# Kernel optimization log

Measured on AMD Instinct MI355X. Metric: run time of the kernel, lower is better.

The kernel has to match this reference:

```python
import jax, jax.numpy as jnp
import numpy as np

NUM_FEATURES = 1024
NUM_GROUPS = 64
NUM_POS = 3
BATCH = 8192  # rows per view; N = NUM_POS * BATCH


def setup_inputs() -> dict:
    key = jax.random.key(0)
    kx, kp = jax.random.split(key)
    x = jax.random.normal(kx, (NUM_POS * BATCH, NUM_FEATURES), dtype=jnp.float32)
    # one independent column permutation per view (deterministic stand-in for torch.randperm)
    pkeys = jax.random.split(kp, NUM_POS)
    perms = jnp.stack([jax.random.permutation(k, NUM_FEATURES) for k in pkeys]).astype(jnp.int32)
    return {"x": x, "perms": perms}


def _group_whiten(x, perms):
    # x: [N, D] with N = 3*B; perms: [3, D]
    N, D = x.shape
    B = N // NUM_POS
    G = NUM_GROUPS
    d = D // G
    xs = x.reshape(NUM_POS, B, D)                                  # [3, B, D]
    # shuffle feature columns per view: x.t()[perm].t()
    xp = jnp.take_along_axis(xs, perms[:, None, :], axis=2)        # [3, B, D]
    xg = xp.reshape(NUM_POS, B, G, d)                              # [3, B, G, d]
    xc = xg - xg.mean(axis=1, keepdims=True)                       # center over batch
    xt = xc.transpose(0, 2, 1, 3)                                  # [3, G, B, d]
    cov = jnp.einsum('sgbd,sgbe->sgde', xt, xt) / B                # [3, G, d, d]
    S, U = jnp.linalg.eigh(cov)                                    # symmetric eig (symeig)
    # W = U diag(S^-1/2) U^T
    W = jnp.einsum('sgde,sge,sgfe->sgdf', U, jax.lax.rsqrt(S), U)  # [3, G, d, d]
    y = jnp.einsum('sgbd,sgde->sgbe', xt, W)                       # [3, G, B, d]
    # unshuffle: transpose(1,2).flatten(0,1)[argsort(perm)].t()
    yf = y.transpose(0, 1, 3, 2).reshape(NUM_POS, D, B)            # [3, D, B]
    inv = jnp.argsort(perms, axis=1)                               # inverse permutation
    yu = jnp.take_along_axis(yf, inv[:, :, None], axis=1)          # [3, D, B]
    return yu.transpose(0, 2, 1).reshape(N, D)                     # [N, D]


def reference(x, perms):
    return _group_whiten(x, perms)
```

## Files before the change

kernel.cpp:

```cpp
#include <hip/hip_runtime.h>
#include <stdint.h>


constexpr int D_FEAT  = 1024;
constexpr int NGROUP  = 64;
constexpr int GD      = 16;
constexpr int NB      = 8192;
constexpr int NVIEW   = 3;

constexpr int P1      = 256;
constexpr int RPP1    = NB / P1;
constexpr int RPB3    = 32;
constexpr int C3      = 4;
constexpr int PSPLIT  = 8;
constexpr int PER     = P1 / PSPLIT;

constexpr int SXX_FLOATS  = NGROUP * GD * GD;
constexpr int PART_STRIDE = SXX_FLOATS + D_FEAT;
constexpr int PSTRIDE_U32 = PART_STRIDE / 2;
constexpr int ENT         = NVIEW * PART_STRIDE;
constexpr int ENT_DW      = NVIEW * PSTRIDE_U32;

constexpr int SX_OFF  = 0;
constexpr int W_OFF   = SX_OFF + NVIEW * D_FEAT;
constexpr int RED_OFF = W_OFF + NVIEW * SXX_FLOATS;

template <int B>
__device__ __forceinline__ float qbc(float x) {
    return __int_as_float(__builtin_amdgcn_mov_dpp(
        __float_as_int(x), B * 0x55 , 0xF, 0xF, true));
}

__device__ __forceinline__ uint32_t pkbf2(float a, float b) {
    uint32_t ua = __float_as_uint(a), ub = __float_as_uint(b);
    ua += 0x7FFFu + ((ua >> 16) & 1u);
    ub += 0x7FFFu + ((ub >> 16) & 1u);
    return (ua >> 16) | (ub & 0xFFFF0000u);
}

__global__ __launch_bounds__(256, 3) void k_stats_gather(const float* __restrict__ x,
                                                         const int* __restrict__ perms,
                                                         uint32_t* __restrict__ part) {
    const int s   = blockIdx.y;
    const int p   = blockIdx.x;
    const int tid = threadIdx.x;

    int pcolq[4];
#pragma unroll
    for (int jj = 0; jj < 4; ++jj) pcolq[jj] = perms[s * D_FEAT + tid * 4 + jj];

    float acc[GD][4];
#pragma unroll
    for (int i = 0; i < GD; ++i)
#pragma unroll
        for (int jj = 0; jj < 4; ++jj) acc[i][jj] = 0.0f;
    float sacc[4] = {0.0f, 0.0f, 0.0f, 0.0f};

    const float* xbase = x + (size_t)(s * NB + p * RPP1) * D_FEAT;

#define ROW_ACC(Q0, Q1, Q2, Q3)                                                \
    {                                                                          \
        float vq_[4] = {Q0, Q1, Q2, Q3};                                       \
        float v_[GD];                                                          \
        _Pragma("unroll")                                                      \
        for (int jj = 0; jj < 4; ++jj) {                                       \
            v_[0  + jj] = qbc<0>(vq_[jj]);                                     \
            v_[4  + jj] = qbc<1>(vq_[jj]);                                     \
            v_[8  + jj] = qbc<2>(vq_[jj]);                                     \
            v_[12 + jj] = qbc<3>(vq_[jj]);                                     \
        }                                                                      \
        _Pragma("unroll")                                                      \
        for (int jj = 0; jj < 4; ++jj) sacc[jj] += vq_[jj];                    \
        _Pragma("unroll")                                                      \
        for (int i = 0; i < GD; ++i)                                           \
            _Pragma("unroll")                                                  \
            for (int jj = 0; jj < 4; ++jj)                                     \
                acc[i][jj] = fmaf(v_[i], vq_[jj], acc[i][jj]);                 \
    }

    for (int r = 0; r < RPP1; r += 4) {
        const float* r0 = xbase + (size_t)r * D_FEAT;
        const float* r1 = r0 + D_FEAT;
        const float* r2 = r1 + D_FEAT;
        const float* r3 = r2 + D_FEAT;
        const float a0 = r0[pcolq[0]], a1 = r0[pcolq[1]],
                    a2 = r0[pcolq[2]], a3 = r0[pcolq[3]];
        const float b0 = r1[pcolq[0]], b1 = r1[pcolq[1]],
                    b2 = r1[pcolq[2]], b3 = r1[pcolq[3]];
        const float c0 = r2[pcolq[0]], c1 = r2[pcolq[1]],
                    c2 = r2[pcolq[2]], c3 = r2[pcolq[3]];
        const float d0 = r3[pcolq[0]], d1 = r3[pcolq[1]],
                    d2 = r3[pcolq[2]], d3 = r3[pcolq[3]];
        ROW_ACC(a0, a1, a2, a3)
        ROW_ACC(b0, b1, b2, b3)
        ROW_ACC(c0, c1, c2, c3)
        ROW_ACC(d0, d1, d2, d3)
    }
#undef ROW_ACC

    uint32_t* dst = part + (size_t)(s * P1 + p) * PSTRIDE_U32;
#pragma unroll
    for (int i = 0; i < GD; ++i) {
        dst[i * 512 + tid * 2 + 0] = pkbf2(acc[i][0], acc[i][1]);
        dst[i * 512 + tid * 2 + 1] = pkbf2(acc[i][2], acc[i][3]);
    }
    dst[8192 + tid * 2 + 0] = pkbf2(sacc[0], sacc[1]);
    dst[8192 + tid * 2 + 1] = pkbf2(sacc[2], sacc[3]);
}

__global__ __launch_bounds__(256) void k_reduce1(const uint32_t* __restrict__ part,
                                                 float* __restrict__ red) {
    const int fd = blockIdx.x * 256 + threadIdx.x;
    if (fd >= ENT_DW) return;
    const int s = fd / PSTRIDE_U32, ffd = fd % PSTRIDE_U32;
    const uint32_t* src =
        part + ((size_t)s * P1 + blockIdx.y * PER) * PSTRIDE_U32 + ffd;
    float s0 = 0.0f, s1 = 0.0f;
#pragma unroll 8
    for (int p = 0; p < PER; ++p) {
        const uint32_t u = src[(size_t)p * PSTRIDE_U32];
        s0 += __uint_as_float(u << 16);
        s1 += __uint_as_float(u & 0xFFFF0000u);
    }
    float* r = red + (size_t)blockIdx.y * ENT + s * PART_STRIDE + ffd * 2;
    r[0] = s0;
    r[1] = s1;
}

__global__ __launch_bounds__(256) void k_invsqrt(const float* __restrict__ red,
                                                 float* __restrict__ ws) {
    __shared__ float Ym[GD][GD];
    __shared__ float Zm[GD][GD];
    __shared__ float Tm[GD][GD];
    __shared__ float Mu[GD];
    const int bx = blockIdx.x;
    const int s = bx >> 6, g = bx & 63;
    const int tid = threadIdx.x;
    const int i = tid >> 4, j = tid & 15;
    const float invB = 1.0f / (float)NB;

    const int f_sxx = s * PART_STRIDE + i * D_FEAT + g * GD + j;
    float sxx = 0.0f;
#pragma unroll
    for (int pp = 0; pp < PSPLIT; ++pp) sxx += red[(size_t)pp * ENT + f_sxx];

    if (tid < GD) {
        const int f_sx = s * PART_STRIDE + SXX_FLOATS + g * GD + tid;
        float sx = 0.0f;
#pragma unroll
        for (int pp = 0; pp < PSPLIT; ++pp) sx += red[(size_t)pp * ENT + f_sx];
        ws[SX_OFF + s * D_FEAT + g * GD + tid] = sx;
        Mu[tid] = sx * invB;
    }
    __syncthreads();
    const float a = sxx * invB - Mu[i] * Mu[j];

    Ym[i][j] = a;
    __syncthreads();
    float tr = 0.0f;
#pragma unroll
    for (int k = 0; k < GD; ++k) tr += Ym[k][k];
    const float sc = tr * (1.0f / (float)GD);
    const float inv_sc = 1.0f / sc;
    __syncthreads();
    Ym[i][j] = a * inv_sc;
    Zm[i][j] = (i == j) ? 1.0f : 0.0f;
    __syncthreads();

    float zn = (i == j) ? 1.0f : 0.0f;
    for (int it = 0; it < 6; ++it) {
        float t = 0.0f;
#pragma unroll
        for (int k = 0; k < GD; ++k) t += Zm[i][k] * Ym[k][j];
        t = ((i == j) ? 1.5f : 0.0f) - 0.5f * t;
        Tm[i][j] = t;
        __syncthreads();
        float yn = 0.0f;
        zn = 0.0f;
#pragma unroll
        for (int k = 0; k < GD; ++k) {
            yn += Ym[i][k] * Tm[k][j];
            zn += Tm[i][k] * Zm[k][j];
        }
        __syncthreads();
        Ym[i][j] = yn;
        Zm[i][j] = zn;
        __syncthreads();
    }
    ws[W_OFF + (size_t)((s * NGROUP + g) * GD + i) * GD + j] = zn * rsqrtf(sc);
}

__global__ __launch_bounds__(256, 3) void k_apply(const float* __restrict__ x,
                                                  const int* __restrict__ perms,
                                                  const float* __restrict__ ws,
                                                  float* __restrict__ out) {
    __shared__ float bin[2][C3][D_FEAT];
    __shared__ float bout[C3][D_FEAT];
    const int s   = blockIdx.y;
    const int rb  = blockIdx.x;
    const int tid = threadIdx.x;
    const int g   = tid >> 2;
    const int q   = tid & 3;
    const float invB = 1.0f / (float)NB;

    int pcolq[4];
#pragma unroll
    for (int jj = 0; jj < 4; ++jj) pcolq[jj] = perms[s * D_FEAT + tid * 4 + jj];

    const float* Wp = ws + W_OFF + (size_t)(s * NGROUP + g) * GD * GD;
    float w[GD][4];
#pragma unroll
    for (int e = 0; e < GD; ++e) {
        float4 t4 = *(const float4*)&Wp[e * GD + q * 4];
        w[e][0] = t4.x; w[e][1] = t4.y; w[e][2] = t4.z; w[e][3] = t4.w;
    }
    float bias[4] = {0.0f, 0.0f, 0.0f, 0.0f};
#pragma unroll
    for (int e = 0; e < GD; ++e) {
        const float mu = ws[SX_OFF + s * D_FEAT + g * GD + e] * invB;
#pragma unroll
        for (int ii = 0; ii < 4; ++ii) bias[ii] += mu * w[e][ii];
    }

    const float* xbase = x + (size_t)(s * NB + rb * RPB3) * D_FEAT;
    float* obase = out + (size_t)(s * NB + rb * RPB3) * D_FEAT;
    constexpr int NCH = RPB3 / C3;

    float4 rr[C3];
#pragma unroll
    for (int t = 0; t < C3; ++t)
        rr[t] = *(const float4*)&xbase[(size_t)t * D_FEAT + tid * 4];

    for (int k = 0; k < NCH; ++k) {
#pragma unroll
        for (int t = 0; t < C3; ++t)
            *(float4*)&bin[k & 1][t][tid * 4] = rr[t];
        __syncthreads();
        if (k + 1 < NCH) {
            const float* nx = xbase + (size_t)(k + 1) * C3 * D_FEAT;
#pragma unroll
            for (int t = 0; t < C3; ++t)
                rr[t] = *(const float4*)&nx[(size_t)t * D_FEAT + tid * 4];
        }
        const float (*cb)[D_FEAT] = bin[k & 1];
#pragma unroll
        for (int r = 0; r < C3; ++r) {
            float vq[4];
#pragma unroll
            for (int jj = 0; jj < 4; ++jj) vq[jj] = cb[r][pcolq[jj]];
            float v[GD];
#pragma unroll
            for (int jj = 0; jj < 4; ++jj) {
                v[0  + jj] = qbc<0>(vq[jj]);
                v[4  + jj] = qbc<1>(vq[jj]);
                v[8  + jj] = qbc<2>(vq[jj]);
                v[12 + jj] = qbc<3>(vq[jj]);
            }
            float u[4] = {-bias[0], -bias[1], -bias[2], -bias[3]};
#pragma unroll
            for (int e = 0; e < GD; ++e)
#pragma unroll
                for (int ii = 0; ii < 4; ++ii) u[ii] = fmaf(v[e], w[e][ii], u[ii]);
#pragma unroll
            for (int ii = 0; ii < 4; ++ii) bout[r][pcolq[ii]] = u[ii];
        }
        __syncthreads();
        float* ob = obase + (size_t)k * C3 * D_FEAT;
#pragma unroll
        for (int t = 0; t < C3; ++t)
            *(float4*)&ob[(size_t)t * D_FEAT + tid * 4] =
                *(const float4*)&bout[t][tid * 4];
    }
}

extern "C" void kernel_launch(void* const* d_in, const int* in_sizes, int n_in,
                              void* d_out, int out_size, void* d_ws, size_t ws_size,
                              hipStream_t stream) {
    const float* x     = (const float*)d_in[0];
    const int*   perms = (const int*)d_in[1];
    float* out = (float*)d_out;
    float* ws  = (float*)d_ws;

    uint32_t* part = (uint32_t*)out;

    dim3 g1(P1, NVIEW);
    k_stats_gather<<<g1, 256, 0, stream>>>(x, perms, part);

    dim3 gr1((ENT_DW + 255) / 256, PSPLIT);
    k_reduce1<<<gr1, 256, 0, stream>>>(part, ws + RED_OFF);

    k_invsqrt<<<NVIEW * NGROUP, 256, 0, stream>>>(ws + RED_OFF, ws);

    dim3 g3(NB / RPB3, NVIEW);
    k_apply<<<g3, 256, 0, stream>>>(x, perms, ws, out);
}
```

Before: 96.75 us.

## Pre-transpose input to bf16 column-major so stats kernel reads contiguous vectors

A new transpose kernel converts each view of x into a column-major layout packed as bf16 pairs, stored in spare space in the output buffer. The statistics kernel then reads 16-byte vectors along the batch for each permuted column instead of doing scattered per-element gathers across rows. This aims for coalesced, vectorised loads and half the bytes in the covariance pass. In exchange it adds a full extra pass over x, reading it and writing a bf16 copy. Covariance inputs also drop from fp32 to bf16 precision.

```diff
diff --git a/kernel.cpp b/kernel.cpp
--- a/kernel.cpp
+++ b/kernel.cpp
@@ -21,6 +21,9 @@
 constexpr int ENT         = NVIEW * PART_STRIDE;
 constexpr int ENT_DW      = NVIEW * PSTRIDE_U32;
 
+constexpr int PART_DW_TOTAL = NVIEW * P1 * PSTRIDE_U32;
+constexpr int XT_OFF_DW     = PART_DW_TOTAL;
+
 constexpr int SX_OFF  = 0;
 constexpr int W_OFF   = SX_OFF + NVIEW * D_FEAT;
 constexpr int RED_OFF = W_OFF + NVIEW * SXX_FLOATS;
@@ -38,7 +41,38 @@
     return (ua >> 16) | (ub & 0xFFFF0000u);
 }
 
-__global__ __launch_bounds__(256, 3) void k_stats_gather(const float* __restrict__ x,
+__global__ __launch_bounds__(256, 4) void k_transpose(const float* __restrict__ x,
+                                                      uint32_t* __restrict__ xt) {
+    __shared__ float tile[64][65];
+    const int s  = blockIdx.z;
+    const int cb = blockIdx.y;
+    const int rb = blockIdx.x;
+    const int tid = threadIdx.x;
+    const int tx = tid & 15, ty = tid >> 4;
+
+    const float* src = x + (size_t)(s * NB + rb * 64) * D_FEAT + cb * 64;
+#pragma unroll
+    for (int i = 0; i < 4; ++i) {
+        const int rl = i * 16 + ty;
+        const float4 v = *(const float4*)&src[(size_t)rl * D_FEAT + tx * 4];
+        tile[rl][tx * 4 + 0] = v.x;
+        tile[rl][tx * 4 + 1] = v.y;
+        tile[rl][tx * 4 + 2] = v.z;
+        tile[rl][tx * 4 + 3] = v.w;
+    }
+    __syncthreads();
+    const int cl = tid >> 2;
+    const int rq = tid & 3;
+    uint32_t pk[8];
+#pragma unroll
+    for (int m = 0; m < 8; ++m)
+        pk[m] = pkbf2(tile[rq * 16 + 2 * m][cl], tile[rq * 16 + 2 * m + 1][cl]);
+    uint32_t* dst = xt + (size_t)(s * D_FEAT + cb * 64 + cl) * 4096 + rb * 32 + rq * 8;
+    *(uint4*)&dst[0] = make_uint4(pk[0], pk[1], pk[2], pk[3]);
+    *(uint4*)&dst[4] = make_uint4(pk[4], pk[5], pk[6], pk[7]);
+}
+
+__global__ __launch_bounds__(256, 3) void k_stats_gather(const uint32_t* __restrict__ xt,
                                                          const int* __restrict__ perms,
                                                          uint32_t* __restrict__ part) {
     const int s   = blockIdx.y;
@@ -56,11 +90,26 @@
         for (int jj = 0; jj < 4; ++jj) acc[i][jj] = 0.0f;
     float sacc[4] = {0.0f, 0.0f, 0.0f, 0.0f};
 
-    const float* xbase = x + (size_t)(s * NB + p * RPP1) * D_FEAT;
-
-#define ROW_ACC(Q0, Q1, Q2, Q3)                                                \
+    const uint4* xt4 = (const uint4*)xt;
+    const size_t b0 = (size_t)(s * D_FEAT + pcolq[0]) * 1024 + p * 4;
+    const size_t b1 = (size_t)(s * D_FEAT + pcolq[1]) * 1024 + p * 4;
+    const size_t b2 = (size_t)(s * D_FEAT + pcolq[2]) * 1024 + p * 4;
+    const size_t b3 = (size_t)(s * D_FEAT + pcolq[3]) * 1024 + p * 4;
+
+#define ROW_ACC_P(D0, D1, D2, D3, LO)                                          \
     {                                                                          \
-        float vq_[4] = {Q0, Q1, Q2, Q3};                                       \
+        float vq_[4];                                                          \
+        if (LO) {                                                              \
+            vq_[0] = __uint_as_float((D0) << 16);                              \
+            vq_[1] = __uint_as_float((D1) << 16);                              \
+            vq_[2] = __uint_as_float((D2) << 16);                              \
+            vq_[3] = __uint_as_float((D3) << 16);                              \
+        } else {                                                               \
+            vq_[0] = __uint_as_float((D0) & 0xFFFF0000u);                      \
+            vq_[1] = __uint_as_float((D1) & 0xFFFF0000u);                      \
+            vq_[2] = __uint_as_float((D2) & 0xFFFF0000u);                      \
+            vq_[3] = __uint_as_float((D3) & 0xFFFF0000u);                      \
+        }                                                                      \
         float v_[GD];                                                          \
         _Pragma("unroll")                                                      \
         for (int jj = 0; jj < 4; ++jj) {                                       \
@@ -78,25 +127,18 @@
                 acc[i][jj] = fmaf(v_[i], vq_[jj], acc[i][jj]);                 \
     }
 
-    for (int r = 0; r < RPP1; r += 4) {
-        const float* r0 = xbase + (size_t)r * D_FEAT;
-        const float* r1 = r0 + D_FEAT;
-        const float* r2 = r1 + D_FEAT;
-        const float* r3 = r2 + D_FEAT;
-        const float a0 = r0[pcolq[0]], a1 = r0[pcolq[1]],
-                    a2 = r0[pcolq[2]], a3 = r0[pcolq[3]];
-        const float b0 = r1[pcolq[0]], b1 = r1[pcolq[1]],
-                    b2 = r1[pcolq[2]], b3 = r1[pcolq[3]];
-        const float c0 = r2[pcolq[0]], c1 = r2[pcolq[1]],
-                    c2 = r2[pcolq[2]], c3 = r2[pcolq[3]];
-        const float d0 = r3[pcolq[0]], d1 = r3[pcolq[1]],
-                    d2 = r3[pcolq[2]], d3 = r3[pcolq[3]];
-        ROW_ACC(a0, a1, a2, a3)
-        ROW_ACC(b0, b1, b2, b3)
-        ROW_ACC(c0, c1, c2, c3)
-        ROW_ACC(d0, d1, d2, d3)
-    }
-#undef ROW_ACC
+#pragma unroll
+    for (int seg = 0; seg < 4; ++seg) {
+        const uint4 U0 = xt4[b0 + seg];
+        const uint4 U1 = xt4[b1 + seg];
+        const uint4 U2 = xt4[b2 + seg];
+        const uint4 U3 = xt4[b3 + seg];
+        ROW_ACC_P(U0.x, U1.x, U2.x, U3.x, 1) ROW_ACC_P(U0.x, U1.x, U2.x, U3.x, 0)
+        ROW_ACC_P(U0.y, U1.y, U2.y, U3.y, 1) ROW_ACC_P(U0.y, U1.y, U2.y, U3.y, 0)
+        ROW_ACC_P(U0.z, U1.z, U2.z, U3.z, 1) ROW_ACC_P(U0.z, U1.z, U2.z, U3.z, 0)
+        ROW_ACC_P(U0.w, U1.w, U2.w, U3.w, 1) ROW_ACC_P(U0.w, U1.w, U2.w, U3.w, 0)
+    }
+#undef ROW_ACC_P
 
     uint32_t* dst = part + (size_t)(s * P1 + p) * PSTRIDE_U32;
 #pragma unroll
@@ -282,9 +324,13 @@
     float* ws  = (float*)d_ws;
 
     uint32_t* part = (uint32_t*)out;
+    uint32_t* xt   = (uint32_t*)out + XT_OFF_DW;
+
+    dim3 gt(NB / 64, D_FEAT / 64, NVIEW);
+    k_transpose<<<gt, 256, 0, stream>>>(x, xt);
 
     dim3 g1(P1, NVIEW);
-    k_stats_gather<<<g1, 256, 0, stream>>>(x, perms, part);
+    k_stats_gather<<<g1, 256, 0, stream>>>(xt, perms, part);
 
     dim3 gr1((ENT_DW + 255) / 256, PSPLIT);
     k_reduce1<<<gr1, 256, 0, stream>>>(part, ws + RED_OFF);
```

Measured after the change: 124.8 us. 1.29x slower.
